# Performance work log

Measured on AMD Instinct MI355X. Metric: run time of the kernel, lower is better.

The kernel has to match this reference:

```python
import jax, jax.numpy as jnp
import numpy as np
from jax import lax

B, L, I, H, O = 4096, 60, 13, 128, 2  # batch, seq len (fixed by Linear), input, hidden, output


def _lstm_dir(x, w_ih, w_hh, b_ih, b_hh, reverse):
    """Single-direction LSTM, PyTorch gate order (i, f, g, o). x: [B, L, In] -> [B, L, H]."""
    Hn = w_hh.shape[1]
    # Precompute input projection for all timesteps: [L, B, 4H]
    xp = jnp.einsum('bli,gi->lbg', x, w_ih) + b_ih + b_hh

    def step(carry, xt):
        h, c = carry
        gates = xt + h @ w_hh.T
        i, f, g, o = jnp.split(gates, 4, axis=-1)
        c = jax.nn.sigmoid(f) * c + jax.nn.sigmoid(i) * jnp.tanh(g)
        h = jax.nn.sigmoid(o) * jnp.tanh(c)
        return (h, c), h

    init = (jnp.zeros((x.shape[0], Hn), x.dtype), jnp.zeros((x.shape[0], Hn), x.dtype))
    _, hs = lax.scan(step, init, xp, reverse=reverse)  # outputs kept in original time order
    return jnp.swapaxes(hs, 0, 1)


def _bilstm(x, wf, hf, bif, bhf, wb, hb, bib, bhb):
    fwd = _lstm_dir(x, wf, hf, bif, bhf, False)
    bwd = _lstm_dir(x, wb, hb, bib, bhb, True)
    return jnp.concatenate([fwd, bwd], axis=-1)  # [B, L, 2H]


def setup_inputs() -> dict:
    key = jax.random.key(0)
    ks = iter(jax.random.split(key, 40))

    def p(shape, s=0.08):
        return jax.random.normal(next(ks), shape, dtype=jnp.float32) * s

    d = {"x": jax.random.normal(next(ks), (B, L, I), dtype=jnp.float32)}
    ins = [I, 2 * H, 2 * H]
    for l in range(3):
        for suf in ("f", "b"):
            d[f"w_ih_{l}{suf}"] = p((4 * H, ins[l]))
            d[f"w_hh_{l}{suf}"] = p((4 * H, H))
            d[f"b_ih_{l}{suf}"] = p((4 * H,))
            d[f"b_hh_{l}{suf}"] = p((4 * H,))
    d["w_out"] = p((O, 2 * H * L))
    d["b_out"] = p((O,))
    return d


def reference(x,
              w_ih_0f, w_hh_0f, b_ih_0f, b_hh_0f, w_ih_0b, w_hh_0b, b_ih_0b, b_hh_0b,
              w_ih_1f, w_hh_1f, b_ih_1f, b_hh_1f, w_ih_1b, w_hh_1b, b_ih_1b, b_hh_1b,
              w_ih_2f, w_hh_2f, b_ih_2f, b_hh_2f, w_ih_2b, w_hh_2b, b_ih_2b, b_hh_2b,
              w_out, b_out):
    y = _bilstm(x, w_ih_0f, w_hh_0f, b_ih_0f, b_hh_0f, w_ih_0b, w_hh_0b, b_ih_0b, b_hh_0b)
    y = _bilstm(y, w_ih_1f, w_hh_1f, b_ih_1f, b_hh_1f, w_ih_1b, w_hh_1b, b_ih_1b, b_hh_1b)
    y = _bilstm(y, w_ih_2f, w_hh_2f, b_ih_2f, b_hh_2f, w_ih_2b, w_hh_2b, b_ih_2b, b_hh_2b)
    y = jax.nn.relu(y.reshape(y.shape[0], -1))  # [B, 2H*L]
    return y @ w_out.T + b_out  # [B, O]
```

## Files before the change

### kernel.cpp

```cpp
#include <hip/hip_runtime.h>
#include <math.h>

#define B_  4096
#define L_  60
#define I_  13
#define H_  128
#define AHP 136

typedef _Float16 half8 __attribute__((ext_vector_type(8)));
typedef _Float16 half4v __attribute__((ext_vector_type(4)));
typedef float float4v __attribute__((ext_vector_type(4)));

__global__ void pack_kernel(const float* __restrict__ src, _Float16* __restrict__ dst,
                            int Ksrc, int n,
                            const float* __restrict__ bih, const float* __restrict__ bhh,
                            float* __restrict__ bias_out) {
    int g0 = blockIdx.x * blockDim.x + threadIdx.x;
    for (int e = g0; e < n; e += gridDim.x * blockDim.x) {
        int j  = e & 7;
        int l  = (e >> 3) & 63;
        int ct = (e >> 9) & 7;
        int w4 = (e >> 12) & 3;
        int kt = e >> 14;
        int nn = (ct >> 1) * 128 + w4 * 32 + (ct & 1) * 16 + (l & 15);
        int k  = kt * 32 + ((l >> 4) << 3) + j;
        dst[e] = (k < Ksrc) ? (_Float16)src[nn * Ksrc + k] : (_Float16)0.f;
    }
    if (bias_out && g0 < 512) bias_out[g0] = bih[g0] + bhh[g0];
}

__device__ __forceinline__ float sigm(float x) {
    return __builtin_amdgcn_rcpf(1.f + __expf(-x));
}
__device__ __forceinline__ float tanh_f(float x) {
    return 1.f - 2.f * __builtin_amdgcn_rcpf(__expf(2.f * x) + 1.f);
}

#define SMEM_HALFS 78080

template <int XT, int IS_L0>
__global__ __launch_bounds__(512)
void lstm_mfma(const float* __restrict__ x0, const _Float16* __restrict__ yin,
               const _Float16* __restrict__ px_f, const _Float16* __restrict__ ph_f,
               const _Float16* __restrict__ px_b, const _Float16* __restrict__ ph_b,
               const float* __restrict__ bias_f, const float* __restrict__ bias_b,
               _Float16* __restrict__ yout)
{
    __shared__ _Float16 sm[SMEM_HALFS];
    _Float16* WH = sm;

    const int tid  = threadIdx.x;
    const int lane = tid & 63;
    const int w    = tid >> 6;
    const int w4   = w & 3;
    const int u    = w >> 2;
    const int dir  = blockIdx.x & 1;
    const int rb   = (blockIdx.x >> 1) * 32;
    const int m    = lane & 15;
    const int q    = lane >> 4;
    const int jc   = w4 * 32 + u * 16 + m;

    const int crow = tid >> 4;
    const int ccg  = tid & 15;
    _Float16* __restrict__ ybase =
        yout + (size_t)(rb + crow) * 15360 + dir * H_ + ccg * 8;

    const _Float16* __restrict__ px   = dir ? px_b : px_f;
    const _Float16* __restrict__ ph   = dir ? ph_b : ph_f;
    const float*    __restrict__ bias = dir ? bias_b : bias_f;
    const _Float16* __restrict__ pWl  = px + w4 * 4096 + u * 512 + lane * 8;
    const _Float16* __restrict__ WHl  = WH + w4 * 4096 + u * 512 + lane * 8;

    {
        const half8* s8 = (const half8*)ph;
        half8* d8 = (half8*)WH;
        for (int i = tid; i < 8192; i += 512) d8[i] = s8[i];
    }

    float bv[4];
#pragma unroll
    for (int tq = 0; tq < 4; ++tq) bv[tq] = bias[tq * 128 + jc];

    if (IS_L0) {
        _Float16* AH0 = sm + 65536;
        _Float16* AH1 = AH0 + 32 * AHP;
        _Float16* AX  = AH1 + 32 * AHP;
        for (int i = tid; i < 2 * 32 * AHP; i += 512) AH0[i] = (_Float16)0.f;

        half8 bX[4];
#pragma unroll
        for (int tq = 0; tq < 4; ++tq) bX[tq] = *(const half8*)(pWl + tq * 1024);

        float cst[2][4];
#pragma unroll
        for (int rt = 0; rt < 2; ++rt)
#pragma unroll
            for (int r = 0; r < 4; ++r) cst[rt][r] = 0.f;

        for (int s = 0; s < L_; ++s) {
            const int t = dir ? (L_ - 1 - s) : s;
            _Float16* __restrict__ Hprev = (s & 1) ? AH0 : AH1;
            _Float16* __restrict__ Hcur  = (s & 1) ? AH1 : AH0;
            _Float16* __restrict__ AXs   = AX + (s & 1) * 1024;

            if (tid < 256) {
                const int e  = tid * 4;
                const int j0 = e & 7;
                const int ln = (e >> 3) & 63;
                const int rt = e >> 9;
                const int row = rt * 16 + (ln & 15);
                const int kb  = ((ln >> 4) << 3) + j0;
                const float* xr = x0 + (size_t)(rb + row) * (L_ * I_) + t * I_;
                half4v tmp;
#pragma unroll
                for (int jj = 0; jj < 4; ++jj) {
                    int k = kb + jj;
                    tmp[jj] = (k < I_) ? (_Float16)xr[k] : (_Float16)0.f;
                }
                ((half4v*)AXs)[tid] = tmp;
            }

            __syncthreads();

            if (s > 0) {
                const int tp = dir ? (t + 1) : (t - 1);
                half8 hv = *(const half8*)(Hprev + crow * AHP + ccg * 8);
                *(half8*)(ybase + tp * 256) = hv;
            }

            float4v acc[2][4];
#pragma unroll
            for (int rt = 0; rt < 2; ++rt)
#pragma unroll
                for (int tq = 0; tq < 4; ++tq) {
                    float b = bv[tq];
                    acc[rt][tq] = (float4v){b, b, b, b};
                }

            {
                half8 a0 = *(const half8*)(AXs + lane * 8);
                half8 a1 = *(const half8*)(AXs + 512 + lane * 8);
#pragma unroll
                for (int tq = 0; tq < 4; ++tq) {
                    acc[0][tq] = __builtin_amdgcn_mfma_f32_16x16x32_f16(a0, bX[tq], acc[0][tq], 0, 0, 0);
                    acc[1][tq] = __builtin_amdgcn_mfma_f32_16x16x32_f16(a1, bX[tq], acc[1][tq], 0, 0, 0);
                }
            }

#pragma unroll
            for (int kh = 0; kh < 4; ++kh) {
                half8 a0 = *(const half8*)(Hprev + m * AHP + kh * 32 + q * 8);
                half8 a1 = *(const half8*)(Hprev + (16 + m) * AHP + kh * 32 + q * 8);
#pragma unroll
                for (int tq = 0; tq < 4; ++tq) {
                    half8 b = *(const half8*)(WHl + kh * 16384 + tq * 1024);
                    acc[0][tq] = __builtin_amdgcn_mfma_f32_16x16x32_f16(a0, b, acc[0][tq], 0, 0, 0);
                    acc[1][tq] = __builtin_amdgcn_mfma_f32_16x16x32_f16(a1, b, acc[1][tq], 0, 0, 0);
                }
            }

#pragma unroll
            for (int rt = 0; rt < 2; ++rt)
#pragma unroll
                for (int r = 0; r < 4; ++r) {
                    const float gi = acc[rt][0][r];
                    const float gf = acc[rt][1][r];
                    const float gg = acc[rt][2][r];
                    const float go = acc[rt][3][r];
                    const float cc = sigm(gf) * cst[rt][r] + sigm(gi) * tanh_f(gg);
                    cst[rt][r] = cc;
                    const float hh = sigm(go) * tanh_f(cc);
                    const int row = rt * 16 + q * 4 + r;
                    Hcur[row * AHP + jc] = (_Float16)hh;
                }
        }
        __syncthreads();
        {
            _Float16* __restrict__ Hl = ((L_ - 1) & 1) ? AH1 : AH0;
            const int tp = dir ? 0 : (L_ - 1);
            half8 hv = *(const half8*)(Hl + crow * AHP + ccg * 8);
            *(half8*)(ybase + tp * 256) = hv;
        }
        return;
    }

    _Float16* AH = sm + 65536;
    _Float16* XS = AH + 32 * AHP;
    for (int i = tid; i < 32 * AHP; i += 512) AH[i] = (_Float16)0.f;

    const int c0 = tid * 2;
    const int f0 = c0 >> 6,       l0 = c0 & 63;
    const int f1 = (c0 + 1) >> 6, l1 = (c0 + 1) & 63;
    const _Float16* __restrict__ sb0 =
        yin + (size_t)(rb + (f0 & 1) * 16 + (l0 & 15)) * 15360 + (f0 >> 1) * 32 + (l0 >> 4) * 8;
    const _Float16* __restrict__ sb1 =
        yin + (size_t)(rb + (f1 & 1) * 16 + (l1 & 15)) * 15360 + (f1 >> 1) * 32 + (l1 >> 4) * 8;
    _Float16* __restrict__ xw = XS + c0 * 8;

    {
        const int t0 = dir ? (L_ - 1) : 0;
        *(half8*)xw       = *(const half8*)(sb0 + t0 * 256);
        *(half8*)(xw + 8) = *(const half8*)(sb1 + t0 * 256);
    }

    float cst[2][4];
#pragma unroll
    for (int rt = 0; rt < 2; ++rt)
#pragma unroll
        for (int r = 0; r < 4; ++r) cst[rt][r] = 0.f;

    __syncthreads();

    for (int s = 0; s < L_; ++s) {
        const int t  = dir ? (L_ - 1 - s) : s;
        const int sn = (s + 1 < L_) ? s + 1 : s;
        const int tn = dir ? (L_ - 1 - sn) : sn;

        half8 sg0 = *(const half8*)(sb0 + tn * 256);
        half8 sg1 = *(const half8*)(sb1 + tn * 256);

        half8 bC[4], bN[4];
#pragma unroll
        for (int tq = 0; tq < 4; ++tq) bC[tq] = *(const half8*)(pWl + tq * 1024);

        if (s > 0) {
            const int tp = dir ? (t + 1) : (t - 1);
            half8 hv = *(const half8*)(AH + crow * AHP + ccg * 8);
            *(half8*)(ybase + tp * 256) = hv;
        }

        float4v acc[2][4];
#pragma unroll
        for (int rt = 0; rt < 2; ++rt)
#pragma unroll
            for (int tq = 0; tq < 4; ++tq) {
                float b = bv[tq];
                acc[rt][tq] = (float4v){b, b, b, b};
            }

#pragma unroll
        for (int kt = 0; kt < XT; ++kt) {
            if (kt + 1 < XT) {
#pragma unroll
                for (int tq = 0; tq < 4; ++tq)
                    bN[tq] = *(const half8*)(pWl + (kt + 1) * 16384 + tq * 1024);
            }
            if ((kt & 1) == 0) {
                const int kh = kt >> 1;
                half8 ha0 = *(const half8*)(AH + m * AHP + kh * 32 + q * 8);
                half8 ha1 = *(const half8*)(AH + (16 + m) * AHP + kh * 32 + q * 8);
#pragma unroll
                for (int tq = 0; tq < 4; ++tq) {
                    half8 hb = *(const half8*)(WHl + kh * 16384 + tq * 1024);
                    acc[0][tq] = __builtin_amdgcn_mfma_f32_16x16x32_f16(ha0, hb, acc[0][tq], 0, 0, 0);
                    acc[1][tq] = __builtin_amdgcn_mfma_f32_16x16x32_f16(ha1, hb, acc[1][tq], 0, 0, 0);
                }
            }
            half8 a0 = *(const half8*)(XS + (kt * 2 + 0) * 512 + lane * 8);
            half8 a1 = *(const half8*)(XS + (kt * 2 + 1) * 512 + lane * 8);
#pragma unroll
            for (int tq = 0; tq < 4; ++tq) {
                acc[0][tq] = __builtin_amdgcn_mfma_f32_16x16x32_f16(a0, bC[tq], acc[0][tq], 0, 0, 0);
                acc[1][tq] = __builtin_amdgcn_mfma_f32_16x16x32_f16(a1, bC[tq], acc[1][tq], 0, 0, 0);
            }
            if (kt + 1 < XT) {
#pragma unroll
                for (int tq = 0; tq < 4; ++tq) bC[tq] = bN[tq];
            }
        }

        _Float16 hh8[2][4];
#pragma unroll
        for (int rt = 0; rt < 2; ++rt)
#pragma unroll
            for (int r = 0; r < 4; ++r) {
                const float gi = acc[rt][0][r];
                const float gf = acc[rt][1][r];
                const float gg = acc[rt][2][r];
                const float go = acc[rt][3][r];
                const float cc = sigm(gf) * cst[rt][r] + sigm(gi) * tanh_f(gg);
                cst[rt][r] = cc;
                hh8[rt][r] = (_Float16)(sigm(go) * tanh_f(cc));
            }

        __syncthreads();

        *(half8*)xw       = sg0;
        *(half8*)(xw + 8) = sg1;
#pragma unroll
        for (int rt = 0; rt < 2; ++rt)
#pragma unroll
            for (int r = 0; r < 4; ++r) {
                const int row = rt * 16 + q * 4 + r;
                AH[row * AHP + jc] = hh8[rt][r];
            }

        __syncthreads();
    }

    {
        const int tp = dir ? 0 : (L_ - 1);
        half8 hv = *(const half8*)(AH + crow * AHP + ccg * 8);
        *(half8*)(ybase + tp * 256) = hv;
    }
}

__global__ __launch_bounds__(256)
void final_kernel(const _Float16* __restrict__ y, const float* __restrict__ wout,
                  const float* __restrict__ bout, float* __restrict__ outp, int nrows) {
    const int wid  = (blockIdx.x * blockDim.x + threadIdx.x) >> 6;
    const int lane = threadIdx.x & 63;
    if (wid >= nrows) return;
    const half8*  __restrict__ y8 = (const half8*)(y + (size_t)wid * 15360);
    const float4* __restrict__ w4 = (const float4*)wout;
    float s0 = 0.f, s1 = 0.f;
#pragma unroll 2
    for (int it = 0; it < 30; ++it) {
        const int idx = it * 64 + lane;
        half8 h = y8[idx];
        float v[8];
#pragma unroll
        for (int e = 0; e < 8; ++e) v[e] = fmaxf((float)h[e], 0.f);
        const float4 a0 = w4[idx * 2], a1 = w4[idx * 2 + 1];
        const float4 b0 = w4[3840 + idx * 2], b1 = w4[3840 + idx * 2 + 1];
        s0 += v[0] * a0.x + v[1] * a0.y + v[2] * a0.z + v[3] * a0.w
            + v[4] * a1.x + v[5] * a1.y + v[6] * a1.z + v[7] * a1.w;
        s1 += v[0] * b0.x + v[1] * b0.y + v[2] * b0.z + v[3] * b0.w
            + v[4] * b1.x + v[5] * b1.y + v[6] * b1.z + v[7] * b1.w;
    }
#pragma unroll
    for (int off = 32; off > 0; off >>= 1) {
        s0 += __shfl_down(s0, off);
        s1 += __shfl_down(s1, off);
    }
    if (lane == 0) {
        outp[wid * 2 + 0] = s0 + bout[0];
        outp[wid * 2 + 1] = s1 + bout[1];
    }
}

extern "C" void kernel_launch(void* const* d_in, const int* in_sizes, int n_in,
                              void* d_out, int out_size, void* d_ws, size_t ws_size,
                              hipStream_t stream) {
    const float* x = (const float*)d_in[0];
    auto W = [&](int l, int d, int which) { return (const float*)d_in[1 + l * 8 + d * 4 + which]; };
    const float* w_out = (const float*)d_in[25];
    const float* b_out = (const float*)d_in[26];

    _Float16* wsH = (_Float16*)d_ws;
    const size_t px0f = 0,       ph0f = 16384;
    const size_t px0b = 81920,   ph0b = 98304;
    const size_t px1f = 163840,  ph1f = 294912;
    const size_t px1b = 360448,  ph1b = 491520;
    const size_t px2f = 557056,  ph2f = 688128;
    const size_t px2b = 753664,  ph2b = 884736;
    const size_t packs_end = 950272;
    float* bias = (float*)(wsH + packs_end);
    const size_t head_bytes = packs_end * 2 + 4096 * 4;
    _Float16* y0 = (_Float16*)((char*)d_ws + head_bytes);

    pack_kernel<<<64, 256, 0, stream>>>(W(0,0,0), wsH + px0f, I_,  16384,  W(0,0,2), W(0,0,3), bias + 0);
    pack_kernel<<<256,256, 0, stream>>>(W(0,0,1), wsH + ph0f, H_,  65536,  nullptr, nullptr, nullptr);
    pack_kernel<<<64, 256, 0, stream>>>(W(0,1,0), wsH + px0b, I_,  16384,  W(0,1,2), W(0,1,3), bias + 512);
    pack_kernel<<<256,256, 0, stream>>>(W(0,1,1), wsH + ph0b, H_,  65536,  nullptr, nullptr, nullptr);
    pack_kernel<<<512,256, 0, stream>>>(W(1,0,0), wsH + px1f, 256, 131072, W(1,0,2), W(1,0,3), bias + 1024);
    pack_kernel<<<256,256, 0, stream>>>(W(1,0,1), wsH + ph1f, H_,  65536,  nullptr, nullptr, nullptr);
    pack_kernel<<<512,256, 0, stream>>>(W(1,1,0), wsH + px1b, 256, 131072, W(1,1,2), W(1,1,3), bias + 1536);
    pack_kernel<<<256,256, 0, stream>>>(W(1,1,1), wsH + ph1b, H_,  65536,  nullptr, nullptr, nullptr);
    pack_kernel<<<512,256, 0, stream>>>(W(2,0,0), wsH + px2f, 256, 131072, W(2,0,2), W(2,0,3), bias + 2048);
    pack_kernel<<<256,256, 0, stream>>>(W(2,0,1), wsH + ph2f, H_,  65536,  nullptr, nullptr, nullptr);
    pack_kernel<<<512,256, 0, stream>>>(W(2,1,0), wsH + px2b, 256, 131072, W(2,1,2), W(2,1,3), bias + 2560);
    pack_kernel<<<256,256, 0, stream>>>(W(2,1,1), wsH + ph2b, H_,  65536,  nullptr, nullptr, nullptr);

    const size_t avail_halfs = (ws_size > head_bytes) ? (ws_size - head_bytes) / 2 : 0;
    int chunks = 1;
    while (chunks < 128 && (size_t)2 * (B_ / chunks) * 15360 > avail_halfs) chunks *= 2;
    const int CB = B_ / chunks;

    _Float16* yA = y0;
    _Float16* yB = y0 + (size_t)CB * 15360;

    for (int c = 0; c < chunks; ++c) {
        const float* xc = x + (size_t)c * CB * (L_ * I_);
        float* outc = (float*)d_out + (size_t)c * CB * 2;
        lstm_mfma<1, 1><<<2 * CB / 32, 512, 0, stream>>>(
            xc, nullptr, wsH + px0f, wsH + ph0f, wsH + px0b, wsH + ph0b, bias + 0, bias + 512, yA);
        lstm_mfma<8, 0><<<2 * CB / 32, 512, 0, stream>>>(
            nullptr, yA, wsH + px1f, wsH + ph1f, wsH + px1b, wsH + ph1b, bias + 1024, bias + 1536, yB);
        lstm_mfma<8, 0><<<2 * CB / 32, 512, 0, stream>>>(
            nullptr, yB, wsH + px2f, wsH + ph2f, wsH + px2b, wsH + ph2b, bias + 2048, bias + 2560, yA);
        final_kernel<<<(CB + 3) / 4, 256, 0, stream>>>(yA, w_out, b_out, outc, CB);
    }
}
```

Measured before the change: 655.9 us.

## Double-buffer hidden state and inputs, read recurrent weights from global

Hidden-state and input staging buffers are double-buffered in LDS, so each timestep needs one barrier instead of two, and h is written directly into the next buffer. The recurrent weight matrix is no longer copied into shared memory; it is read from global memory (L2) inside the step loop, shrinking the LDS footprint. This trades fewer barriers and less LDS for more global or L2 load latency on the serial critical path.

```diff
diff --git a/kernel.cpp b/kernel.cpp
--- a/kernel.cpp
+++ b/kernel.cpp
@@ -36,7 +36,7 @@
     return 1.f - 2.f * __builtin_amdgcn_rcpf(__expf(2.f * x) + 1.f);
 }
 
-#define SMEM_HALFS 78080
+#define SMEM_HALFS (2 * 32 * AHP + 2 * 8192)
 
 template <int XT, int IS_L0>
 __global__ __launch_bounds__(512)
@@ -47,7 +47,9 @@
                _Float16* __restrict__ yout)
 {
     __shared__ _Float16 sm[SMEM_HALFS];
-    _Float16* WH = sm;
+    _Float16* AH0 = sm;
+    _Float16* AH1 = sm + 32 * AHP;
+    _Float16* XSb = sm + 2 * 32 * AHP;
 
     const int tid  = threadIdx.x;
     const int lane = tid & 63;
@@ -69,23 +71,16 @@
     const _Float16* __restrict__ ph   = dir ? ph_b : ph_f;
     const float*    __restrict__ bias = dir ? bias_b : bias_f;
     const _Float16* __restrict__ pWl  = px + w4 * 4096 + u * 512 + lane * 8;
-    const _Float16* __restrict__ WHl  = WH + w4 * 4096 + u * 512 + lane * 8;
-
-    {
-        const half8* s8 = (const half8*)ph;
-        half8* d8 = (half8*)WH;
-        for (int i = tid; i < 8192; i += 512) d8[i] = s8[i];
-    }
+    const _Float16* __restrict__ WHl  = ph + w4 * 4096 + u * 512 + lane * 8;
+
+    for (int i = tid; i < 2 * 32 * AHP; i += 512) AH0[i] = (_Float16)0.f;
 
     float bv[4];
 #pragma unroll
     for (int tq = 0; tq < 4; ++tq) bv[tq] = bias[tq * 128 + jc];
 
     if (IS_L0) {
-        _Float16* AH0 = sm + 65536;
-        _Float16* AH1 = AH0 + 32 * AHP;
-        _Float16* AX  = AH1 + 32 * AHP;
-        for (int i = tid; i < 2 * 32 * AHP; i += 512) AH0[i] = (_Float16)0.f;
+        _Float16* AX = XSb;
 
         half8 bX[4];
 #pragma unroll
@@ -184,10 +179,6 @@
         return;
     }
 
-    _Float16* AH = sm + 65536;
-    _Float16* XS = AH + 32 * AHP;
-    for (int i = tid; i < 32 * AHP; i += 512) AH[i] = (_Float16)0.f;
-
     const int c0 = tid * 2;
     const int f0 = c0 >> 6,       l0 = c0 & 63;
     const int f1 = (c0 + 1) >> 6, l1 = (c0 + 1) & 63;
@@ -195,10 +186,10 @@
         yin + (size_t)(rb + (f0 & 1) * 16 + (l0 & 15)) * 15360 + (f0 >> 1) * 32 + (l0 >> 4) * 8;
     const _Float16* __restrict__ sb1 =
         yin + (size_t)(rb + (f1 & 1) * 16 + (l1 & 15)) * 15360 + (f1 >> 1) * 32 + (l1 >> 4) * 8;
-    _Float16* __restrict__ xw = XS + c0 * 8;
 
     {
         const int t0 = dir ? (L_ - 1) : 0;
+        _Float16* xw = XSb + c0 * 8;
         *(half8*)xw       = *(const half8*)(sb0 + t0 * 256);
         *(half8*)(xw + 8) = *(const half8*)(sb1 + t0 * 256);
     }
@@ -215,19 +206,23 @@
         const int t  = dir ? (L_ - 1 - s) : s;
         const int sn = (s + 1 < L_) ? s + 1 : s;
         const int tn = dir ? (L_ - 1 - sn) : sn;
+        _Float16* __restrict__ Hprev = (s & 1) ? AH0 : AH1;
+        _Float16* __restrict__ Hcur  = (s & 1) ? AH1 : AH0;
+        const _Float16* __restrict__ XSs = XSb + (s & 1) * 8192;
+        _Float16* __restrict__ XSn = XSb + ((s + 1) & 1) * 8192;
 
         half8 sg0 = *(const half8*)(sb0 + tn * 256);
         half8 sg1 = *(const half8*)(sb1 + tn * 256);
 
-        half8 bC[4], bN[4];
-#pragma unroll
-        for (int tq = 0; tq < 4; ++tq) bC[tq] = *(const half8*)(pWl + tq * 1024);
-
         if (s > 0) {
             const int tp = dir ? (t + 1) : (t - 1);
-            half8 hv = *(const half8*)(AH + crow * AHP + ccg * 8);
+            half8 hv = *(const half8*)(Hprev + crow * AHP + ccg * 8);
             *(half8*)(ybase + tp * 256) = hv;
         }
+
+        half8 bC[4], bN[4];
+#pragma unroll
+        for (int tq = 0; tq < 4; ++tq) bC[tq] = *(const half8*)(pWl + tq * 1024);
 
         float4v acc[2][4];
 #pragma unroll
@@ -247,8 +242,8 @@
             }
             if ((kt & 1) == 0) {
                 const int kh = kt >> 1;
-                half8 ha0 = *(const half8*)(AH + m * AHP + kh * 32 + q * 8);
-                half8 ha1 = *(const half8*)(AH + (16 + m) * AHP + kh * 32 + q * 8);
+                half8 ha0 = *(const half8*)(Hprev + m * AHP + kh * 32 + q * 8);
+                half8 ha1 = *(const half8*)(Hprev + (16 + m) * AHP + kh * 32 + q * 8);
 #pragma unroll
                 for (int tq = 0; tq < 4; ++tq) {
                     half8 hb = *(const half8*)(WHl + kh * 16384 + tq * 1024);
@@ -256,8 +251,8 @@
                     acc[1][tq] = __builtin_amdgcn_mfma_f32_16x16x32_f16(ha1, hb, acc[1][tq], 0, 0, 0);
                 }
             }
-            half8 a0 = *(const half8*)(XS + (kt * 2 + 0) * 512 + lane * 8);
-            half8 a1 = *(const half8*)(XS + (kt * 2 + 1) * 512 + lane * 8);
+            half8 a0 = *(const half8*)(XSs + (kt * 2 + 0) * 512 + lane * 8);
+            half8 a1 = *(const half8*)(XSs + (kt * 2 + 1) * 512 + lane * 8);
 #pragma unroll
             for (int tq = 0; tq < 4; ++tq) {
                 acc[0][tq] = __builtin_amdgcn_mfma_f32_16x16x32_f16(a0, bC[tq], acc[0][tq], 0, 0, 0);
@@ -269,7 +264,8 @@
             }
         }
 
-        _Float16 hh8[2][4];
+        *(half8*)(XSn + c0 * 8)     = sg0;
+        *(half8*)(XSn + c0 * 8 + 8) = sg1;
 #pragma unroll
         for (int rt = 0; rt < 2; ++rt)
 #pragma unroll
@@ -280,27 +276,18 @@
                 const float go = acc[rt][3][r];
                 const float cc = sigm(gf) * cst[rt][r] + sigm(gi) * tanh_f(gg);
                 cst[rt][r] = cc;
-                hh8[rt][r] = (_Float16)(sigm(go) * tanh_f(cc));
+                const float hh = sigm(go) * tanh_f(cc);
+                const int row = rt * 16 + q * 4 + r;
+                Hcur[row * AHP + jc] = (_Float16)hh;
             }
 
         __syncthreads();
-
-        *(half8*)xw       = sg0;
-        *(half8*)(xw + 8) = sg1;
-#pragma unroll
-        for (int rt = 0; rt < 2; ++rt)
-#pragma unroll
-            for (int r = 0; r < 4; ++r) {
-                const int row = rt * 16 + q * 4 + r;
-                AH[row * AHP + jc] = hh8[rt][r];
-            }
-
-        __syncthreads();
     }
 
     {
+        _Float16* __restrict__ Hl = ((L_ - 1) & 1) ? AH1 : AH0;
         const int tp = dir ? 0 : (L_ - 1);
-        half8 hv = *(const half8*)(AH + crow * AHP + ccg * 8);
+        half8 hv = *(const half8*)(Hl + crow * AHP + ccg * 8);
         *(half8*)(ybase + tp * 256) = hv;
     }
 }
```

After: 855.9 us. 30.5% more time.
